# Kernel optimization log

Hardware: AMD Instinct MI355X
Metric: run time of the kernel (lower is better)

## Reference

```python
import jax, jax.numpy as jnp
import numpy as np

MAX_P = 20
MAX_N = 50
FDIM = 256
SCALE = 0.08
STEPS = 3


def _grid_sample_border(feat_hwc, grid):
    # feat_hwc: [B,H,W,C]; grid: [B,Q,2] normalized xy in [-1,1]
    # Bilinear grid_sample, padding_mode='border', align_corners=False (matches torch).
    B, H, W, C = feat_hwc.shape

    def one(fm, g):  # fm [H,W,C], g [Q,2]
        ix = jnp.clip(((g[:, 0] + 1.0) * W - 1.0) * 0.5, 0.0, W - 1.0)
        iy = jnp.clip(((g[:, 1] + 1.0) * H - 1.0) * 0.5, 0.0, H - 1.0)
        x0f = jnp.floor(ix); y0f = jnp.floor(iy)
        wx = (ix - x0f)[:, None]; wy = (iy - y0f)[:, None]
        x0 = x0f.astype(jnp.int32); y0 = y0f.astype(jnp.int32)
        x1 = jnp.minimum(x0 + 1, W - 1); y1 = jnp.minimum(y0 + 1, H - 1)
        f00 = fm[y0, x0]; f01 = fm[y0, x1]  # [Q,C]
        f10 = fm[y1, x0]; f11 = fm[y1, x1]
        top = f00 * (1.0 - wx) + f01 * wx
        bot = f10 * (1.0 - wx) + f11 * wx
        return top * (1.0 - wy) + bot * wy

    return jax.vmap(one)(feat_hwc, grid)


def setup_inputs() -> dict:
    key = jax.random.key(0)
    ks = jax.random.split(key, 12)
    d = {
        'p2': jax.random.normal(ks[0], (4, 256, 256, 256), jnp.float32),
        'p4': jax.random.normal(ks[1], (4, 256, 64, 64), jnp.float32),
        'iw1': jax.random.normal(ks[2], (16384, 512), jnp.float32) * 0.01,
        'ib1': jnp.zeros((512,), jnp.float32),
        'iw2': jax.random.normal(ks[3], (512, 1024), jnp.float32) * 0.04,
        'ib2': jnp.zeros((1024,), jnp.float32),
        'iw3': jax.random.normal(ks[4], (1024, 2000), jnp.float32) * 0.03,
        'ib3': jnp.zeros((2000,), jnp.float32),
        'rw1': jax.random.normal(ks[5], (258, 256), jnp.float32) * 0.06,
        'rb1': jnp.zeros((256,), jnp.float32),
        'rw2': jax.random.normal(ks[6], (256, 128), jnp.float32) * 0.06,
        'rb2': jnp.zeros((128,), jnp.float32),
        'rw3': jax.random.normal(ks[7], (128, 2), jnp.float32) * 0.09,
        'rb3': jnp.zeros((2,), jnp.float32),
        'vw1': jax.random.normal(ks[8], (100, 128), jnp.float32) * 0.1,
        'vb1': jnp.zeros((128,), jnp.float32),
        'vw2': jax.random.normal(ks[9], (128, 1), jnp.float32) * 0.09,
        'vb2': jnp.zeros((1,), jnp.float32),
    }
    return d


def reference(p2, p4, iw1, ib1, iw2, ib2, iw3, ib3,
              rw1, rb1, rw2, rb2, rw3, rb3, vw1, vb1, vw2, vb2):
    B = p4.shape[0]
    # AdaptiveAvgPool2d(8) on 64x64 -> mean over 8x8 blocks
    pooled = p4.reshape(B, FDIM, 8, 8, 8, 8).mean(axis=(3, 5))  # [B,C,8,8]
    flat = pooled.reshape(B, -1)  # [B, C*64]
    h = jax.nn.relu(flat @ iw1 + ib1)
    h = jax.nn.relu(h @ iw2 + ib2)
    init_polygons = jax.nn.sigmoid(h @ iw3 + ib3).reshape(B, MAX_P, MAX_N, 2)

    feat_hwc = jnp.transpose(p2, (0, 2, 3, 1))  # [B,H,W,C]
    polygons = init_polygons
    for _ in range(STEPS):
        coords = polygons.reshape(B, -1, 2)           # [B,Q,2] in [0,1]
        grid = coords * 2.0 - 1.0
        sampled = _grid_sample_border(feat_hwc, grid)  # [B,Q,C]
        inp = jnp.concatenate([sampled, coords], axis=-1)  # [B,Q,C+2]
        r = jax.nn.relu(inp @ rw1 + rb1)
        r = jax.nn.relu(r @ rw2 + rb2)
        disp = jnp.tanh(r @ rw3 + rb3).reshape(B, MAX_P, MAX_N, 2)
        bad = ~jnp.all(jnp.isfinite(disp))
        disp = jnp.where(bad, 0.0,
                         jnp.clip(disp * SCALE, -2.0 * SCALE, 2.0 * SCALE))
        polygons = jnp.clip(polygons + disp, 0.0, 1.0)

    poly_flat = polygons.reshape(B * MAX_P, MAX_N * 2)
    v = jax.nn.relu(poly_flat @ vw1 + vb1)
    validity = jax.nn.sigmoid(v @ vw2 + vb2).reshape(B, MAX_P)
    return polygons, validity, init_polygons
```

## Files before the change

kernel.cpp:

```cpp
#include <hip/hip_runtime.h>
#include <math.h>

#define WS_FLAT 0
#define WS_PART 65536
#define WS_H1   (65536 + 524288)
#define WS_H2   (WS_H1 + 2048)
#define WS_POLY (WS_H2 + 4096)
#define WS_P2T  1048576

__global__ void __launch_bounds__(256) transpose_k(const float* __restrict__ in,
                                                   float* __restrict__ out) {
    __shared__ float t[64][65];
    int tile = blockIdx.x;
    int b  = tile >> 12;
    int ct = (tile >> 10) & 3;
    int xt = tile & 1023;
    int c0 = ct << 6, yx0 = xt << 6;
    int tid = threadIdx.x;

    int jv = (tid & 15) << 2;
    int i0 = tid >> 4;
    const float* ip = in + (((size_t)(b * 256 + c0)) << 16) + yx0;
    #pragma unroll
    for (int ii = i0; ii < 64; ii += 16) {
        float4 v = *(const float4*)(ip + ((size_t)ii << 16) + jv);
        t[jv + 0][ii] = v.x; t[jv + 1][ii] = v.y;
        t[jv + 2][ii] = v.z; t[jv + 3][ii] = v.w;
    }
    __syncthreads();

    int iv = (tid & 15) << 2;
    int j0 = tid >> 4;
    float* op = out + ((size_t)b << 24) + ((size_t)yx0 << 8) + c0;
    #pragma unroll
    for (int jj = j0; jj < 64; jj += 16) {
        float4 v = make_float4(t[jj][iv], t[jj][iv + 1], t[jj][iv + 2], t[jj][iv + 3]);
        *(float4*)(op + ((size_t)jj << 8) + iv) = v;
    }
}

__global__ void pool_k(const float* __restrict__ p4, float* __restrict__ flat) {
    int o = blockIdx.x * blockDim.x + threadIdx.x;
    int b = o >> 14;
    int c = (o >> 6) & 255;
    int ij = o & 63;
    int i = ij >> 3, j = ij & 7;
    const float* base = p4 + (((size_t)(b * 256 + c) * 64 + i * 8) * 64 + j * 8);
    float s = 0.f;
    #pragma unroll
    for (int u = 0; u < 8; ++u) {
        const float4* r = (const float4*)(base + u * 64);
        float4 a = r[0], bb = r[1];
        s += a.x + a.y + a.z + a.w + bb.x + bb.y + bb.z + bb.w;
    }
    flat[o] = s * (1.0f / 64.0f);
}

__global__ void g1a_k(const float* __restrict__ flat, const float* __restrict__ iw1,
                      float* __restrict__ part) {
    __shared__ float sf[4][64];
    int tid = threadIdx.x;
    int kbase = blockIdx.x * 64;
    if (tid < 256) sf[tid >> 6][tid & 63] = flat[(tid >> 6) * 16384 + kbase + (tid & 63)];
    __syncthreads();
    float a0 = 0.f, a1 = 0.f, a2 = 0.f, a3 = 0.f;
    for (int k = 0; k < 64; ++k) {
        float w = iw1[(size_t)(kbase + k) * 512 + tid];
        a0 = fmaf(sf[0][k], w, a0);
        a1 = fmaf(sf[1][k], w, a1);
        a2 = fmaf(sf[2][k], w, a2);
        a3 = fmaf(sf[3][k], w, a3);
    }
    float* pp = part + (size_t)blockIdx.x * 2048;
    pp[tid] = a0; pp[512 + tid] = a1; pp[1024 + tid] = a2; pp[1536 + tid] = a3;
}

__global__ void g1b_k(const float* __restrict__ part, const float* __restrict__ ib1,
                      float* __restrict__ h1) {
    __shared__ float red[8][32];
    int tid = threadIdx.x;
    int cc = tid >> 5, oo = tid & 31;
    int o = blockIdx.x * 32 + oo;
    float s = 0.f;
    for (int i = 0; i < 32; ++i)
        s += part[(size_t)(cc + 8 * i) * 2048 + o];
    red[cc][oo] = s;
    __syncthreads();
    if (cc == 0) {
        float t = 0.f;
        #pragma unroll
        for (int c2 = 0; c2 < 8; ++c2) t += red[c2][oo];
        t += ib1[o & 511];
        h1[o] = fmaxf(t, 0.f);
    }
}

__global__ void g2_k(const float* __restrict__ h1, const float* __restrict__ iw2,
                     const float* __restrict__ ib2, float* __restrict__ h2) {
    __shared__ float sh[512];
    __shared__ float red[4][64];
    int tid = threadIdx.x;
    int b = blockIdx.x >> 4, jt = blockIdx.x & 15;
    sh[tid] = h1[b * 512 + tid];
    sh[tid + 256] = h1[b * 512 + 256 + tid];
    __syncthreads();
    int j = (jt << 6) + (tid & 63);
    int kc = tid >> 6;
    float acc = 0.f;
    for (int k = kc * 128; k < kc * 128 + 128; ++k)
        acc = fmaf(sh[k], iw2[(size_t)k * 1024 + j], acc);
    red[kc][tid & 63] = acc;
    __syncthreads();
    if (kc == 0) {
        float t = red[0][tid] + red[1][tid] + red[2][tid] + red[3][tid] + ib2[j];
        h2[b * 1024 + j] = fmaxf(t, 0.f);
    }
}

__global__ void g3_k(const float* __restrict__ h2, const float* __restrict__ iw3,
                     const float* __restrict__ ib3, float* __restrict__ out_init,
                     float* __restrict__ poly) {
    __shared__ float sh[1024];
    __shared__ float red[4][64];
    int tid = threadIdx.x;
    int b = blockIdx.x >> 5, jt = blockIdx.x & 31;
    const float* h = h2 + b * 1024;
    sh[tid] = h[tid]; sh[tid + 256] = h[tid + 256];
    sh[tid + 512] = h[tid + 512]; sh[tid + 768] = h[tid + 768];
    __syncthreads();
    int j = (jt << 6) + (tid & 63);
    int kc = tid >> 6;
    float acc = 0.f;
    if (j < 2000) {
        for (int k = kc * 256; k < kc * 256 + 256; ++k)
            acc = fmaf(sh[k], iw3[(size_t)k * 2000 + j], acc);
    }
    red[kc][tid & 63] = acc;
    __syncthreads();
    if (kc == 0 && j < 2000) {
        float t = red[0][tid] + red[1][tid] + red[2][tid] + red[3][tid] + ib3[j];
        float s = 1.f / (1.f + expf(-t));
        int o = b * 2000 + j;
        out_init[o] = s;
        poly[o] = s;
    }
}

__global__ void __launch_bounds__(256) step_k(
    const float* __restrict__ p2t,
    const float* __restrict__ rw1, const float* __restrict__ rb1,
    const float* __restrict__ rw2, const float* __restrict__ rb2,
    const float* __restrict__ rw3, const float* __restrict__ rb3,
    float* __restrict__ poly) {
    __shared__ __align__(16) float s_inp[258 * 8];
    __shared__ __align__(16) float s_r1[256 * 8];
    __shared__ __align__(16) float s_r2[128 * 8];
    int tid = threadIdx.x;
    int pt0 = blockIdx.x * 8;
    int b = pt0 / 1000;
    const float* bt = p2t + ((size_t)b << 24);

    float val[8];
    #pragma unroll
    for (int pp = 0; pp < 8; ++pp) {
        int pt = pt0 + pp;
        float cx = poly[pt * 2], cy = poly[pt * 2 + 1];
        float ix = fminf(fmaxf(cx * 256.f - 0.5f, 0.f), 255.f);
        float iy = fminf(fmaxf(cy * 256.f - 0.5f, 0.f), 255.f);
        float x0f = floorf(ix), y0f = floorf(iy);
        int x0 = (int)x0f, y0 = (int)y0f;
        int x1 = min(x0 + 1, 255), y1 = min(y0 + 1, 255);
        float wx = ix - x0f, wy = iy - y0f;
        int r0 = (y0 << 16) + (x0 << 8);
        int r1i = (y1 << 16) + (x0 << 8);
        int dx = (x1 - x0) << 8;
        float f00 = bt[r0 + tid],  f01 = bt[r0 + dx + tid];
        float f10 = bt[r1i + tid], f11 = bt[r1i + dx + tid];
        float top = f00 * (1.f - wx) + f01 * wx;
        float bot = f10 * (1.f - wx) + f11 * wx;
        val[pp] = top * (1.f - wy) + bot * wy;
    }
    ((float4*)&s_inp[tid * 8])[0] = make_float4(val[0], val[1], val[2], val[3]);
    ((float4*)&s_inp[tid * 8])[1] = make_float4(val[4], val[5], val[6], val[7]);
    if (tid < 16) {
        int p = tid >> 1, d = tid & 1;
        s_inp[(256 + d) * 8 + p] = poly[(pt0 + p) * 2 + d];
    }
    __syncthreads();

    {
        float bias = rb1[tid];
        float a0 = bias, a1 = bias, a2 = bias, a3 = bias;
        float a4 = bias, a5 = bias, a6 = bias, a7 = bias;
        for (int k = 0; k < 258; ++k) {
            float w = rw1[k * 256 + tid];
            float4 v0 = ((const float4*)&s_inp[k * 8])[0];
            float4 v1 = ((const float4*)&s_inp[k * 8])[1];
            a0 = fmaf(v0.x, w, a0); a1 = fmaf(v0.y, w, a1);
            a2 = fmaf(v0.z, w, a2); a3 = fmaf(v0.w, w, a3);
            a4 = fmaf(v1.x, w, a4); a5 = fmaf(v1.y, w, a5);
            a6 = fmaf(v1.z, w, a6); a7 = fmaf(v1.w, w, a7);
        }
        ((float4*)&s_r1[tid * 8])[0] =
            make_float4(fmaxf(a0, 0.f), fmaxf(a1, 0.f), fmaxf(a2, 0.f), fmaxf(a3, 0.f));
        ((float4*)&s_r1[tid * 8])[1] =
            make_float4(fmaxf(a4, 0.f), fmaxf(a5, 0.f), fmaxf(a6, 0.f), fmaxf(a7, 0.f));
    }
    __syncthreads();

    {
        int j = tid & 127, ph = tid >> 7;
        float bias = rb2[j];
        float c0 = bias, c1 = bias, c2 = bias, c3 = bias;
        for (int k = 0; k < 256; ++k) {
            float w = rw2[k * 128 + j];
            float4 v = ((const float4*)&s_r1[k * 8])[ph];
            c0 = fmaf(v.x, w, c0); c1 = fmaf(v.y, w, c1);
            c2 = fmaf(v.z, w, c2); c3 = fmaf(v.w, w, c3);
        }
        ((float4*)&s_r2[j * 8])[ph] =
            make_float4(fmaxf(c0, 0.f), fmaxf(c1, 0.f), fmaxf(c2, 0.f), fmaxf(c3, 0.f));
    }
    __syncthreads();

    if (tid < 16) {
        int p = tid >> 1, d = tid & 1;
        float acc = rb3[d];
        for (int k = 0; k < 128; ++k)
            acc = fmaf(s_r2[k * 8 + p], rw3[k * 2 + d], acc);
        float disp = tanhf(acc) * 0.08f;
        disp = fminf(fmaxf(disp, -0.16f), 0.16f);
        int idx = (pt0 + p) * 2 + d;
        float nv = poly[idx] + disp;
        poly[idx] = fminf(fmaxf(nv, 0.f), 1.f);
    }
}

__global__ void valid_k(const float* __restrict__ poly,
                        const float* __restrict__ vw1, const float* __restrict__ vb1,
                        const float* __restrict__ vw2, const float* __restrict__ vb2,
                        float* __restrict__ out) {
    __shared__ float sp[100];
    __shared__ float sred[2];
    int tid = threadIdx.x;
    int row = blockIdx.x;
    if (tid < 100) {
        float v = poly[row * 100 + tid];
        sp[tid] = v;
        out[row * 100 + tid] = v;
    }
    __syncthreads();
    float acc = vb1[tid];
    for (int k = 0; k < 100; ++k)
        acc = fmaf(sp[k], vw1[k * 128 + tid], acc);
    float pr = fmaxf(acc, 0.f) * vw2[tid];
    #pragma unroll
    for (int off = 32; off > 0; off >>= 1)
        pr += __shfl_down(pr, off, 64);
    if ((tid & 63) == 0) sred[tid >> 6] = pr;
    __syncthreads();
    if (tid == 0) {
        float s = sred[0] + sred[1] + vb2[0];
        out[8000 + row] = 1.f / (1.f + expf(-s));
    }
}

extern "C" void kernel_launch(void* const* d_in, const int* in_sizes, int n_in,
                              void* d_out, int out_size, void* d_ws, size_t ws_size,
                              hipStream_t stream) {
    const float* p2  = (const float*)d_in[0];
    const float* p4  = (const float*)d_in[1];
    const float* iw1 = (const float*)d_in[2];
    const float* ib1 = (const float*)d_in[3];
    const float* iw2 = (const float*)d_in[4];
    const float* ib2 = (const float*)d_in[5];
    const float* iw3 = (const float*)d_in[6];
    const float* ib3 = (const float*)d_in[7];
    const float* rw1 = (const float*)d_in[8];
    const float* rb1 = (const float*)d_in[9];
    const float* rw2 = (const float*)d_in[10];
    const float* rb2 = (const float*)d_in[11];
    const float* rw3 = (const float*)d_in[12];
    const float* rb3 = (const float*)d_in[13];
    const float* vw1 = (const float*)d_in[14];
    const float* vb1 = (const float*)d_in[15];
    const float* vw2 = (const float*)d_in[16];
    const float* vb2 = (const float*)d_in[17];
    float* out = (float*)d_out;
    float* ws = (float*)d_ws;
    float* flat = ws + WS_FLAT;
    float* part = ws + WS_PART;
    float* h1   = ws + WS_H1;
    float* h2   = ws + WS_H2;
    float* poly = ws + WS_POLY;
    float* p2t  = ws + WS_P2T;

    pool_k<<<256, 256, 0, stream>>>(p4, flat);
    g1a_k<<<256, 512, 0, stream>>>(flat, iw1, part);
    g1b_k<<<64, 256, 0, stream>>>(part, ib1, h1);
    g2_k<<<64, 256, 0, stream>>>(h1, iw2, ib2, h2);
    g3_k<<<128, 256, 0, stream>>>(h2, iw3, ib3, out + 8080, poly);
    transpose_k<<<16384, 256, 0, stream>>>(p2, p2t);
    for (int s = 0; s < 3; ++s)
        step_k<<<500, 256, 0, stream>>>(p2t, rw1, rb1, rw2, rb2, rw3, rb3, poly);
    valid_k<<<80, 128, 0, stream>>>(poly, vw1, vb1, vw2, vb2, out);
}
```

Baseline: 603.9 us.

## Store transposed feature map in fp16 and register-tile refinement MLP over 16 points

The transpose kernel now writes the channels-last copy of p2 as fp16 instead of fp32, halving the write traffic of the large transpose and the gather traffic in each refinement step. The step kernel handles 16 points per block, using half the blocks. Its two MLP layers are register-tiled as 4 outputs by 4 points per thread with float4 weight loads, so each weight load is reused across more points. This trades fp16 rounding of the sampled features for less memory traffic, and lowers the block count, which may reduce parallelism in the step kernel.

```diff
diff --git a/kernel.cpp b/kernel.cpp
--- a/kernel.cpp
+++ b/kernel.cpp
@@ -1,4 +1,5 @@
 #include <hip/hip_runtime.h>
+#include <hip/hip_fp16.h>
 #include <math.h>
 
 #define WS_FLAT 0
@@ -9,7 +10,7 @@
 #define WS_P2T  1048576
 
 __global__ void __launch_bounds__(256) transpose_k(const float* __restrict__ in,
-                                                   float* __restrict__ out) {
+                                                   __half* __restrict__ out) {
     __shared__ float t[64][65];
     int tile = blockIdx.x;
     int b  = tile >> 12;
@@ -29,13 +30,13 @@
     }
     __syncthreads();
 
-    int iv = (tid & 15) << 2;
-    int j0 = tid >> 4;
-    float* op = out + ((size_t)b << 24) + ((size_t)yx0 << 8) + c0;
+    int cl = (tid & 7) << 3;
     #pragma unroll
-    for (int jj = j0; jj < 64; jj += 16) {
-        float4 v = make_float4(t[jj][iv], t[jj][iv + 1], t[jj][iv + 2], t[jj][iv + 3]);
-        *(float4*)(op + ((size_t)jj << 8) + iv) = v;
+    for (int jj = tid >> 3; jj < 64; jj += 32) {
+        union { __half h[8]; float4 f; } u;
+        #pragma unroll
+        for (int q = 0; q < 8; ++q) u.h[q] = __float2half(t[jj][cl + q]);
+        *(float4*)(out + ((size_t)b << 24) + ((size_t)(yx0 + jj) << 8) + c0 + cl) = u.f;
     }
 }
 
@@ -147,87 +148,116 @@
 }
 
 __global__ void __launch_bounds__(256) step_k(
-    const float* __restrict__ p2t,
+    const __half* __restrict__ p2th,
     const float* __restrict__ rw1, const float* __restrict__ rb1,
     const float* __restrict__ rw2, const float* __restrict__ rb2,
     const float* __restrict__ rw3, const float* __restrict__ rb3,
     float* __restrict__ poly) {
-    __shared__ __align__(16) float s_inp[258 * 8];
-    __shared__ __align__(16) float s_r1[256 * 8];
-    __shared__ __align__(16) float s_r2[128 * 8];
-    int tid = threadIdx.x;
-    int pt0 = blockIdx.x * 8;
-    int b = pt0 / 1000;
-    const float* bt = p2t + ((size_t)b << 24);
-
-    float val[8];
-    #pragma unroll
-    for (int pp = 0; pp < 8; ++pp) {
-        int pt = pt0 + pp;
-        float cx = poly[pt * 2], cy = poly[pt * 2 + 1];
-        float ix = fminf(fmaxf(cx * 256.f - 0.5f, 0.f), 255.f);
-        float iy = fminf(fmaxf(cy * 256.f - 0.5f, 0.f), 255.f);
-        float x0f = floorf(ix), y0f = floorf(iy);
-        int x0 = (int)x0f, y0 = (int)y0f;
-        int x1 = min(x0 + 1, 255), y1 = min(y0 + 1, 255);
-        float wx = ix - x0f, wy = iy - y0f;
-        int r0 = (y0 << 16) + (x0 << 8);
-        int r1i = (y1 << 16) + (x0 << 8);
-        int dx = (x1 - x0) << 8;
-        float f00 = bt[r0 + tid],  f01 = bt[r0 + dx + tid];
-        float f10 = bt[r1i + tid], f11 = bt[r1i + dx + tid];
-        float top = f00 * (1.f - wx) + f01 * wx;
-        float bot = f10 * (1.f - wx) + f11 * wx;
-        val[pp] = top * (1.f - wy) + bot * wy;
-    }
-    ((float4*)&s_inp[tid * 8])[0] = make_float4(val[0], val[1], val[2], val[3]);
-    ((float4*)&s_inp[tid * 8])[1] = make_float4(val[4], val[5], val[6], val[7]);
-    if (tid < 16) {
-        int p = tid >> 1, d = tid & 1;
-        s_inp[(256 + d) * 8 + p] = poly[(pt0 + p) * 2 + d];
-    }
-    __syncthreads();
+    __shared__ __align__(16) float s_inp[258 * 16];
+    __shared__ __align__(16) float s_r1[256 * 16];
+    __shared__ __align__(16) float s_r2[128 * 16];
+    int tid = threadIdx.x;
+    int pt0 = blockIdx.x * 16;
 
     {
-        float bias = rb1[tid];
-        float a0 = bias, a1 = bias, a2 = bias, a3 = bias;
-        float a4 = bias, a5 = bias, a6 = bias, a7 = bias;
+        int ch2 = (tid & 127) << 1;
+        int pgg = tid >> 7;
+        float v0[8], v1[8];
+        #pragma unroll
+        for (int pp = 0; pp < 8; ++pp) {
+            int pt = pt0 + pgg * 8 + pp;
+            int b = pt / 1000;
+            float cx = poly[pt * 2], cy = poly[pt * 2 + 1];
+            float ix = fminf(fmaxf(cx * 256.f - 0.5f, 0.f), 255.f);
+            float iy = fminf(fmaxf(cy * 256.f - 0.5f, 0.f), 255.f);
+            float x0f = floorf(ix), y0f = floorf(iy);
+            int x0 = (int)x0f, y0 = (int)y0f;
+            int x1 = min(x0 + 1, 255), y1 = min(y0 + 1, 255);
+            float wx = ix - x0f, wy = iy - y0f;
+            const __half* bt = p2th + ((size_t)b << 24);
+            int r0 = (y0 << 16) + (x0 << 8) + ch2;
+            int r1a = (y1 << 16) + (x0 << 8) + ch2;
+            int dx = (x1 - x0) << 8;
+            float2 f00 = __half22float2(*(const __half2*)(bt + r0));
+            float2 f01 = __half22float2(*(const __half2*)(bt + r0 + dx));
+            float2 f10 = __half22float2(*(const __half2*)(bt + r1a));
+            float2 f11 = __half22float2(*(const __half2*)(bt + r1a + dx));
+            float t0 = f00.x + (f01.x - f00.x) * wx;
+            float b0 = f10.x + (f11.x - f10.x) * wx;
+            float t1 = f00.y + (f01.y - f00.y) * wx;
+            float b1 = f10.y + (f11.y - f10.y) * wx;
+            v0[pp] = t0 + (b0 - t0) * wy;
+            v1[pp] = t1 + (b1 - t1) * wy;
+        }
+        float* r0p = &s_inp[ch2 * 16 + pgg * 8];
+        float* r1p = &s_inp[(ch2 + 1) * 16 + pgg * 8];
+        ((float4*)r0p)[0] = make_float4(v0[0], v0[1], v0[2], v0[3]);
+        ((float4*)r0p)[1] = make_float4(v0[4], v0[5], v0[6], v0[7]);
+        ((float4*)r1p)[0] = make_float4(v1[0], v1[1], v1[2], v1[3]);
+        ((float4*)r1p)[1] = make_float4(v1[4], v1[5], v1[6], v1[7]);
+        if (tid < 32) {
+            int p = tid >> 1, d = tid & 1;
+            s_inp[(256 + d) * 16 + p] = poly[(pt0 + p) * 2 + d];
+        }
+    }
+    __syncthreads();
+
+    int jc = tid & 63, pg = tid >> 6;
+    {
+        float4 bias = *(const float4*)(rb1 + jc * 4);
+        float4 acc0 = bias, acc1 = bias, acc2 = bias, acc3 = bias;
         for (int k = 0; k < 258; ++k) {
-            float w = rw1[k * 256 + tid];
-            float4 v0 = ((const float4*)&s_inp[k * 8])[0];
-            float4 v1 = ((const float4*)&s_inp[k * 8])[1];
-            a0 = fmaf(v0.x, w, a0); a1 = fmaf(v0.y, w, a1);
-            a2 = fmaf(v0.z, w, a2); a3 = fmaf(v0.w, w, a3);
-            a4 = fmaf(v1.x, w, a4); a5 = fmaf(v1.y, w, a5);
-            a6 = fmaf(v1.z, w, a6); a7 = fmaf(v1.w, w, a7);
+            float4 a = *(const float4*)&s_inp[k * 16 + pg * 4];
+            float4 w = *(const float4*)(rw1 + k * 256 + jc * 4);
+            acc0.x = fmaf(a.x, w.x, acc0.x); acc0.y = fmaf(a.x, w.y, acc0.y);
+            acc0.z = fmaf(a.x, w.z, acc0.z); acc0.w = fmaf(a.x, w.w, acc0.w);
+            acc1.x = fmaf(a.y, w.x, acc1.x); acc1.y = fmaf(a.y, w.y, acc1.y);
+            acc1.z = fmaf(a.y, w.z, acc1.z); acc1.w = fmaf(a.y, w.w, acc1.w);
+            acc2.x = fmaf(a.z, w.x, acc2.x); acc2.y = fmaf(a.z, w.y, acc2.y);
+            acc2.z = fmaf(a.z, w.z, acc2.z); acc2.w = fmaf(a.z, w.w, acc2.w);
+            acc3.x = fmaf(a.w, w.x, acc3.x); acc3.y = fmaf(a.w, w.y, acc3.y);
+            acc3.z = fmaf(a.w, w.z, acc3.z); acc3.w = fmaf(a.w, w.w, acc3.w);
         }
-        ((float4*)&s_r1[tid * 8])[0] =
-            make_float4(fmaxf(a0, 0.f), fmaxf(a1, 0.f), fmaxf(a2, 0.f), fmaxf(a3, 0.f));
-        ((float4*)&s_r1[tid * 8])[1] =
-            make_float4(fmaxf(a4, 0.f), fmaxf(a5, 0.f), fmaxf(a6, 0.f), fmaxf(a7, 0.f));
+        acc0.x = fmaxf(acc0.x, 0.f); acc0.y = fmaxf(acc0.y, 0.f);
+        acc0.z = fmaxf(acc0.z, 0.f); acc0.w = fmaxf(acc0.w, 0.f);
+        acc1.x = fmaxf(acc1.x, 0.f); acc1.y = fmaxf(acc1.y, 0.f);
+        acc1.z = fmaxf(acc1.z, 0.f); acc1.w = fmaxf(acc1.w, 0.f);
+        acc2.x = fmaxf(acc2.x, 0.f); acc2.y = fmaxf(acc2.y, 0.f);
+        acc2.z = fmaxf(acc2.z, 0.f); acc2.w = fmaxf(acc2.w, 0.f);
+        acc3.x = fmaxf(acc3.x, 0.f); acc3.y = fmaxf(acc3.y, 0.f);
+        acc3.z = fmaxf(acc3.z, 0.f); acc3.w = fmaxf(acc3.w, 0.f);
+        *(float4*)&s_r1[(jc * 4 + 0) * 16 + pg * 4] = make_float4(acc0.x, acc1.x, acc2.x, acc3.x);
+        *(float4*)&s_r1[(jc * 4 + 1) * 16 + pg * 4] = make_float4(acc0.y, acc1.y, acc2.y, acc3.y);
+        *(float4*)&s_r1[(jc * 4 + 2) * 16 + pg * 4] = make_float4(acc0.z, acc1.z, acc2.z, acc3.z);
+        *(float4*)&s_r1[(jc * 4 + 3) * 16 + pg * 4] = make_float4(acc0.w, acc1.w, acc2.w, acc3.w);
     }
     __syncthreads();
 
     {
-        int j = tid & 127, ph = tid >> 7;
-        float bias = rb2[j];
-        float c0 = bias, c1 = bias, c2 = bias, c3 = bias;
+        float2 bias = *(const float2*)(rb2 + jc * 2);
+        float2 d0 = bias, d1 = bias, d2 = bias, d3 = bias;
         for (int k = 0; k < 256; ++k) {
-            float w = rw2[k * 128 + j];
-            float4 v = ((const float4*)&s_r1[k * 8])[ph];
-            c0 = fmaf(v.x, w, c0); c1 = fmaf(v.y, w, c1);
-            c2 = fmaf(v.z, w, c2); c3 = fmaf(v.w, w, c3);
+            float4 a = *(const float4*)&s_r1[k * 16 + pg * 4];
+            float2 w = *(const float2*)(rw2 + k * 128 + jc * 2);
+            d0.x = fmaf(a.x, w.x, d0.x); d0.y = fmaf(a.x, w.y, d0.y);
+            d1.x = fmaf(a.y, w.x, d1.x); d1.y = fmaf(a.y, w.y, d1.y);
+            d2.x = fmaf(a.z, w.x, d2.x); d2.y = fmaf(a.z, w.y, d2.y);
+            d3.x = fmaf(a.w, w.x, d3.x); d3.y = fmaf(a.w, w.y, d3.y);
         }
-        ((float4*)&s_r2[j * 8])[ph] =
-            make_float4(fmaxf(c0, 0.f), fmaxf(c1, 0.f), fmaxf(c2, 0.f), fmaxf(c3, 0.f));
-    }
-    __syncthreads();
-
-    if (tid < 16) {
+        d0.x = fmaxf(d0.x, 0.f); d0.y = fmaxf(d0.y, 0.f);
+        d1.x = fmaxf(d1.x, 0.f); d1.y = fmaxf(d1.y, 0.f);
+        d2.x = fmaxf(d2.x, 0.f); d2.y = fmaxf(d2.y, 0.f);
+        d3.x = fmaxf(d3.x, 0.f); d3.y = fmaxf(d3.y, 0.f);
+        *(float4*)&s_r2[(jc * 2 + 0) * 16 + pg * 4] = make_float4(d0.x, d1.x, d2.x, d3.x);
+        *(float4*)&s_r2[(jc * 2 + 1) * 16 + pg * 4] = make_float4(d0.y, d1.y, d2.y, d3.y);
+    }
+    __syncthreads();
+
+    if (tid < 32) {
         int p = tid >> 1, d = tid & 1;
         float acc = rb3[d];
         for (int k = 0; k < 128; ++k)
-            acc = fmaf(s_r2[k * 8 + p], rw3[k * 2 + d], acc);
+            acc = fmaf(s_r2[k * 16 + p], rw3[k * 2 + d], acc);
         float disp = tanhf(acc) * 0.08f;
         disp = fminf(fmaxf(disp, -0.16f), 0.16f);
         int idx = (pt0 + p) * 2 + d;
@@ -293,15 +323,15 @@
     float* h1   = ws + WS_H1;
     float* h2   = ws + WS_H2;
     float* poly = ws + WS_POLY;
-    float* p2t  = ws + WS_P2T;
+    __half* p2th = (__half*)(ws + WS_P2T);
 
     pool_k<<<256, 256, 0, stream>>>(p4, flat);
     g1a_k<<<256, 512, 0, stream>>>(flat, iw1, part);
     g1b_k<<<64, 256, 0, stream>>>(part, ib1, h1);
     g2_k<<<64, 256, 0, stream>>>(h1, iw2, ib2, h2);
     g3_k<<<128, 256, 0, stream>>>(h2, iw3, ib3, out + 8080, poly);
-    transpose_k<<<16384, 256, 0, stream>>>(p2, p2t);
+    transpose_k<<<16384, 256, 0, stream>>>(p2, p2th);
     for (int s = 0; s < 3; ++s)
-        step_k<<<500, 256, 0, stream>>>(p2t, rw1, rb1, rw2, rb2, rw3, rb3, poly);
+        step_k<<<250, 256, 0, stream>>>(p2th, rw1, rb1, rw2, rb2, rw3, rb3, poly);
     valid_k<<<80, 128, 0, stream>>>(poly, vw1, vb1, vw2, vb2, out);
 }
```

After: 585.0 us. -3.1%, faster.
